# Kernel tuning notes

Measured on AMD Instinct MI355X. Metric: run time of the kernel, lower is better.

The kernel has to match this reference:

```python
import jax, jax.numpy as jnp
import numpy as np

N_NODES = 100000
N_EDGES = 3200000
N_FEAT = 128
EMBED = 20
N_CLASSES = 10
N_GRAPHS = 64


def setup_inputs() -> dict:
    key = jax.random.key(0)
    ks = jax.random.split(key, 8)
    x = jax.random.normal(ks[0], (N_NODES, N_FEAT), dtype=jnp.float32)
    edge_index = jax.random.randint(ks[1], (2, N_EDGES), 0, N_NODES, dtype=jnp.int64)
    edge_weights = jax.random.uniform(ks[2], (N_EDGES,), dtype=jnp.float32)
    batch = jnp.sort(jax.random.randint(ks[3], (N_NODES,), 0, N_GRAPHS, dtype=jnp.int64))
    # GCNConv parameters (glorot-ish scale) and final linear layer
    W = jax.random.normal(ks[4], (N_FEAT, EMBED), dtype=jnp.float32) * (1.0 / np.sqrt(N_FEAT))
    b = jnp.zeros((EMBED,), dtype=jnp.float32)
    lin_W = jax.random.normal(ks[5], (2 * EMBED, N_CLASSES), dtype=jnp.float32) * (1.0 / np.sqrt(2 * EMBED))
    lin_b = jnp.zeros((N_CLASSES,), dtype=jnp.float32)
    return {"x": x, "edge_index": edge_index, "edge_weights": edge_weights,
            "batch": batch, "W": W, "b": b, "lin_W": lin_W, "lin_b": lin_b}


def reference(x, edge_index, edge_weights, batch, W, b, lin_W, lin_b):
    N = x.shape[0]
    # --- GCNConv with self-loops and symmetric normalization (PyG semantics) ---
    loops = jnp.arange(N, dtype=edge_index.dtype)
    src = jnp.concatenate([edge_index[0], loops])
    dst = jnp.concatenate([edge_index[1], loops])
    w = jnp.concatenate([edge_weights, jnp.ones((N,), dtype=edge_weights.dtype)])
    deg = jax.ops.segment_sum(w, dst, num_segments=N)  # degree at targets
    dinv = jnp.where(deg > 0, jax.lax.rsqrt(deg), 0.0)
    norm = dinv[src] * w * dinv[dst]  # [E+N]
    xw = x @ W  # [N, EMBED]
    msg = xw[src] * norm[:, None]  # gather + scale
    out1 = jax.ops.segment_sum(msg, dst, num_segments=N) + b  # scatter-add
    # --- L2 normalize per node (F.normalize p=2 dim=1, eps=1e-12), then ReLU ---
    nrm = jnp.sqrt(jnp.sum(out1 * out1, axis=1, keepdims=True))
    embed = jax.nn.relu(out1 / jnp.maximum(nrm, 1e-12))
    # --- global max / mean pool per graph ---
    mx = jax.ops.segment_max(embed, batch, num_segments=N_GRAPHS)
    mx = jnp.where(jnp.isfinite(mx), mx, 0.0)  # empty graphs -> 0
    cnt = jax.ops.segment_sum(jnp.ones((N,), dtype=embed.dtype), batch, num_segments=N_GRAPHS)
    mean = jax.ops.segment_sum(embed, batch, num_segments=N_GRAPHS) / jnp.maximum(cnt, 1.0)[:, None]
    pooled = jnp.concatenate([mx, mean], axis=-1)  # [G, 2*EMBED]
    return pooled @ lin_W + lin_b
```

## Files before the change

kernel.cpp:

```cpp
#include <hip/hip_runtime.h>
#include <hip/hip_fp16.h>

#define NN 100000
#define NE 3200000
#define NF 128
#define EM 20
#define NC 10
#define NG 64

#define NB 782
#define CAPB 4608
#define T 4096
#define SBLK 1024
#define NXW 391

__global__ __launch_bounds__(SBLK) void k_scatfat(
        const int* __restrict__ src, const int* __restrict__ dst,
        const float* __restrict__ w, int* __restrict__ gcursor,
        uint2* __restrict__ barr,
        const float* __restrict__ x, const float* __restrict__ W,
        float* __restrict__ xwf) {
    __shared__ __align__(16) char smem[52352];
    int tid = threadIdx.x;

    if (blockIdx.x < NXW) {
        float* Ws = (float*)smem;
        for (int i = tid; i < NF * EM; i += SBLK) Ws[i] = W[i];
        __syncthreads();
        int node = blockIdx.x * 256 + (tid >> 2);
        int j0 = (tid & 3) * 5;
        if (node >= NN) return;
        float acc[5] = {0.f, 0.f, 0.f, 0.f, 0.f};
        const float4* xr = (const float4*)(x + (size_t)node * NF);
        for (int k4 = 0; k4 < NF / 4; ++k4) {
            float4 xc = xr[k4];
            const float* wr = Ws + (k4 * 4) * EM + j0;
#pragma unroll
            for (int jj = 0; jj < 5; ++jj) acc[jj] = fmaf(xc.x, wr[jj], acc[jj]);
            wr += EM;
#pragma unroll
            for (int jj = 0; jj < 5; ++jj) acc[jj] = fmaf(xc.y, wr[jj], acc[jj]);
            wr += EM;
#pragma unroll
            for (int jj = 0; jj < 5; ++jj) acc[jj] = fmaf(xc.z, wr[jj], acc[jj]);
            wr += EM;
#pragma unroll
            for (int jj = 0; jj < 5; ++jj) acc[jj] = fmaf(xc.w, wr[jj], acc[jj]);
        }
        float* o = xwf + (size_t)node * EM + j0;
#pragma unroll
        for (int jj = 0; jj < 5; ++jj) o[jj] = acc[jj];
        return;
    }

    unsigned int* cnt   = (unsigned int*)smem;
    unsigned int* off   = (unsigned int*)(smem + 4096);
    unsigned int* gbase = (unsigned int*)(smem + 8192);
    unsigned int* wsum  = (unsigned int*)(smem + 11320);
    uint2*        staged= (uint2*)(smem + 11384);
    unsigned short* bkt = (unsigned short*)(smem + 44152);

    long E0 = (long)(blockIdx.x - NXW) * T;
    int tot = (int)min((long)T, (long)NE - E0);
    cnt[tid] = 0;
    __syncthreads();
    unsigned int dreg[T / SBLK];
#pragma unroll
    for (int k = 0; k < T / SBLK; ++k) {
        int e = k * SBLK + tid;
        dreg[k] = 0;
        if (e < tot) {
            dreg[k] = (unsigned)dst[E0 + e];
            atomicAdd(&cnt[dreg[k] >> 7], 1u);
        }
    }
    __syncthreads();
    {
        int lane = tid & 63, wv = tid >> 6;
        unsigned int v = cnt[tid];
        unsigned int s = v;
#pragma unroll
        for (int o = 1; o < 64; o <<= 1) {
            unsigned int t = __shfl_up(s, o);
            if (lane >= o) s += t;
        }
        if (lane == 63) wsum[wv] = s;
        __syncthreads();
        if (tid == 0) {
            unsigned int a = 0;
#pragma unroll
            for (int i = 0; i < 16; ++i) { unsigned int t = wsum[i]; wsum[i] = a; a += t; }
        }
        __syncthreads();
        off[tid] = wsum[wv] + s - v;
    }
    __syncthreads();
    if (tid < NB) {
        unsigned int c = cnt[tid];
        gbase[tid] = c ? (unsigned int)atomicAdd(&gcursor[tid], (int)c) : 0u;
        cnt[tid] = 0;
    }
    __syncthreads();
#pragma unroll
    for (int k = 0; k < T / SBLK; ++k) {
        int e = k * SBLK + tid;
        if (e < tot) {
            long ge = E0 + e;
            unsigned int d = dreg[k];
            unsigned int b = d >> 7;
            unsigned int slot = atomicAdd(&cnt[b], 1u);
            unsigned int pos = off[b] + slot;
            staged[pos] = make_uint2((((unsigned)src[ge]) << 7) | (d & 127u),
                                     __float_as_uint(w[ge]));
            bkt[pos] = (unsigned short)b;
        }
    }
    __syncthreads();
    for (int i = tid; i < tot; i += SBLK) {
        unsigned int b = bkt[i];
        unsigned int gpos = gbase[b] + ((unsigned)i - off[b]);
        if (gpos < CAPB) barr[(size_t)b * CAPB + gpos] = staged[i];
    }
}

__global__ __launch_bounds__(1024) void k_degps(
        const int* __restrict__ gcursor, const uint2* __restrict__ barr,
        const float* xwf, float* __restrict__ dinv,
        __half* __restrict__ xwhA, __half* __restrict__ xwhB) {
    __shared__ float dacc[128];
    __shared__ float dvs[128];
    int bk = blockIdx.x, tid = threadIdx.x;
    if (tid < 128) dacc[tid] = 0.f;
    __syncthreads();
    int cntb = min(gcursor[bk], CAPB);
    const uint2* row = barr + (size_t)bk * CAPB;
    for (int i = tid; i < cntb; i += 1024) {
        uint2 r = row[i];
        atomicAdd(&dacc[r.x & 127u], __uint_as_float(r.y));
    }
    __syncthreads();
    if (tid < 128) {
        float dv = rsqrtf(1.0f + dacc[tid]);
        dvs[tid] = dv;
        int gd = bk * 128 + tid;
        if (gd < NN) dinv[gd] = dv;
    }
    __syncthreads();
    for (int i = tid; i < 128 * EM; i += 1024) {
        int n = i / EM, dim = i - n * EM;
        int gd = bk * 128 + n;
        if (gd < NN) {
            __half hv = __float2half(xwf[(size_t)gd * EM + dim] * dvs[n]);
            if (dim < 16) xwhA[(size_t)gd * 16 + dim] = hv;
            else          xwhB[(size_t)gd * 4 + (dim - 16)] = hv;
        }
    }
}

__device__ inline void unpack16(uint4 a0, uint4 a1, float* f) {
    const __half2* h = (const __half2*)&a0;
#pragma unroll
    for (int c = 0; c < 4; ++c) { float2 t = __half22float2(h[c]); f[2*c] = t.x; f[2*c+1] = t.y; }
    h = (const __half2*)&a1;
#pragma unroll
    for (int c = 0; c < 4; ++c) { float2 t = __half22float2(h[c]); f[8+2*c] = t.x; f[9+2*c] = t.y; }
}
__device__ inline void unpack4(uint2 b0, float* f) {
    const __half2* h = (const __half2*)&b0;
#pragma unroll
    for (int c = 0; c < 2; ++c) { float2 t = __half22float2(h[c]); f[2*c] = t.x; f[2*c+1] = t.y; }
}

__global__ void k_sortaggr(const int* __restrict__ gcursor,
                           const unsigned long long* __restrict__ barr64,
                           const __half* __restrict__ xwhA, const __half* __restrict__ xwhB,
                           const float* __restrict__ dinv, const float* __restrict__ b,
                           float* embed) {
    __shared__ unsigned long long srt[CAPB];
    __shared__ unsigned int cnt[128];
    __shared__ unsigned int off[128];
    __shared__ unsigned int wtot;
    int bk = blockIdx.x, tid = threadIdx.x;
    if (tid < 128) cnt[tid] = 0;
    __syncthreads();
    int cntb = min(gcursor[bk], CAPB);
    const unsigned long long* row = barr64 + (size_t)bk * CAPB;
    unsigned long long rec[9];
    unsigned int pos[9];
    int K = 0;
    for (int e = tid; e < cntb; e += 512) {
        rec[K] = row[e];
        pos[K] = atomicAdd(&cnt[(unsigned)rec[K] & 127u], 1u);
        ++K;
    }
    __syncthreads();
    unsigned int v = 0, s = 0;
    if (tid < 128) {
        v = cnt[tid]; s = v;
#pragma unroll
        for (int o = 1; o < 64; o <<= 1) {
            unsigned int t = __shfl_up(s, o);
            if ((tid & 63) >= o) s += t;
        }
        if (tid == 63) wtot = s;
    }
    __syncthreads();
    if (tid < 128) {
        if (tid >= 64) s += wtot;
        off[tid] = s;
    }
    __syncthreads();
    for (int k = 0; k < K; ++k) {
        unsigned int dl = (unsigned)rec[k] & 127u;
        srt[off[dl] - cnt[dl] + pos[k]] = rec[k];
    }
    __syncthreads();
    int d = tid >> 2, sub = tid & 3;
    int s0 = (int)(off[d] - cnt[d]), s1 = (int)off[d];
    const uint4* pA = (const uint4*)xwhA;
    const uint2* pB = (const uint2*)xwhB;
    float acc[20];
#pragma unroll
    for (int j = 0; j < 20; ++j) acc[j] = 0.f;
    for (int e = s0 + sub; e < s1; e += 4) {
        unsigned long long r = srt[e];
        unsigned int sN = ((unsigned int)r) >> 7;
        float nw = __uint_as_float((unsigned int)(r >> 32));
        uint4 a0 = pA[(size_t)sN * 2];
        uint4 a1 = pA[(size_t)sN * 2 + 1];
        uint2 b0 = pB[sN];
        float f[20];
        unpack16(a0, a1, f);
        unpack4(b0, f + 16);
#pragma unroll
        for (int j = 0; j < 20; ++j) acc[j] = fmaf(f[j], nw, acc[j]);
    }
#pragma unroll
    for (int j = 0; j < 20; ++j) {
        acc[j] += __shfl_xor(acc[j], 1);
        acc[j] += __shfl_xor(acc[j], 2);
    }
    if (sub == 0) {
        int gd = bk * 128 + d;
        if (gd < NN) {
            float dv = dinv[gd];
            uint4 a0 = pA[(size_t)gd * 2];
            uint4 a1 = pA[(size_t)gd * 2 + 1];
            uint2 b0 = pB[gd];
            float xdh[20];
            unpack16(a0, a1, xdh);
            unpack4(b0, xdh + 16);
            float r[20];
            float ss = 0.f;
#pragma unroll
            for (int j = 0; j < 20; ++j) {
                r[j] = dv * (acc[j] + xdh[j]) + b[j];
                ss = fmaf(r[j], r[j], ss);
            }
            float inv = 1.0f / fmaxf(sqrtf(ss), 1e-12f);
            float4 o4[5];
            float* o = (float*)o4;
#pragma unroll
            for (int j = 0; j < 20; ++j) {
                float e2 = r[j] * inv;
                o[j] = e2 > 0.f ? e2 : 0.f;
            }
            float4* eo = (float4*)(embed + (size_t)gd * EM);
#pragma unroll
            for (int c = 0; c < 5; ++c) eo[c] = o4[c];
        }
    }
}

__device__ inline int lbound(const int* __restrict__ batch, int key) {
    int lo = 0, hi = NN;
    while (lo < hi) {
        int mid = (lo + hi) >> 1;
        if (batch[mid] < key) lo = mid + 1; else hi = mid;
    }
    return lo;
}

__global__ void k_poolfinal(const float* __restrict__ embed, const int* __restrict__ batch,
                            const float* __restrict__ lw, const float* __restrict__ lb,
                            float* __restrict__ out) {
    __shared__ float cross[4][40];
    __shared__ float pooled[40];
    int g = blockIdx.x;
    int s0 = lbound(batch, g), s1 = lbound(batch, g + 1);
    int cnt = s1 - s0;
    float mx[EM], sm[EM];
#pragma unroll
    for (int j = 0; j < EM; ++j) { mx[j] = 0.f; sm[j] = 0.f; }
    for (int n = s0 + threadIdx.x; n < s1; n += 256) {
        const float4* e = (const float4*)(embed + (size_t)n * EM);
#pragma unroll
        for (int c = 0; c < 5; ++c) {
            float4 v = e[c];
            int j = c * 4;
            mx[j+0] = fmaxf(mx[j+0], v.x); sm[j+0] += v.x;
            mx[j+1] = fmaxf(mx[j+1], v.y); sm[j+1] += v.y;
            mx[j+2] = fmaxf(mx[j+2], v.z); sm[j+2] += v.z;
            mx[j+3] = fmaxf(mx[j+3], v.w); sm[j+3] += v.w;
        }
    }
#pragma unroll
    for (int o = 32; o > 0; o >>= 1) {
#pragma unroll
        for (int j = 0; j < EM; ++j) {
            mx[j] = fmaxf(mx[j], __shfl_xor(mx[j], o));
            sm[j] += __shfl_xor(sm[j], o);
        }
    }
    int wave = threadIdx.x >> 6, lane = threadIdx.x & 63;
    if (lane == 0) {
#pragma unroll
        for (int j = 0; j < EM; ++j) { cross[wave][j] = mx[j]; cross[wave][EM + j] = sm[j]; }
    }
    __syncthreads();
    if (threadIdx.x < 40) {
        int j = threadIdx.x;
        float v = cross[0][j];
        if (j < EM) v = fmaxf(fmaxf(v, cross[1][j]), fmaxf(cross[2][j], cross[3][j]));
        else        v = v + cross[1][j] + cross[2][j] + cross[3][j];
        if (j >= EM) v *= 1.0f / fmaxf((float)cnt, 1.0f);
        pooled[j] = v;
    }
    __syncthreads();
    if (threadIdx.x < NC) {
        int c = threadIdx.x;
        float acc = lb[c];
#pragma unroll
        for (int j = 0; j < 2 * EM; ++j) acc = fmaf(pooled[j], lw[j * NC + c], acc);
        out[g * NC + c] = acc;
    }
}

static inline size_t align_up(size_t v) { return (v + 1023) & ~(size_t)1023; }

extern "C" void kernel_launch(void* const* d_in, const int* in_sizes, int n_in,
                              void* d_out, int out_size, void* d_ws, size_t ws_size,
                              hipStream_t stream) {
    const float* x     = (const float*)d_in[0];
    const int*   ei    = (const int*)d_in[1];
    const float* ew    = (const float*)d_in[2];
    const int*   batch = (const int*)d_in[3];
    const float* W     = (const float*)d_in[4];
    const float* b     = (const float*)d_in[5];
    const float* lw    = (const float*)d_in[6];
    const float* lb    = (const float*)d_in[7];
    float* out = (float*)d_out;

    char* ws = (char*)d_ws;
    int*    gcursor = (int*)ws;    ws += align_up(4096);
    float*  dinv    = (float*)ws;  ws += align_up((size_t)NN * 4);
    __half* xwhA    = (__half*)ws; ws += align_up((size_t)NN * 16 * 2);
    __half* xwhB    = (__half*)ws; ws += align_up((size_t)NN * 4 * 2);
    float*  xwf     = (float*)ws;  ws += align_up((size_t)NN * EM * 4);
    uint2*  barr    = (uint2*)ws;
    unsigned long long* barr64 = (unsigned long long*)barr;
    float*  embed   = xwf;

    const int* srcp = ei;
    const int* dstp = ei + NE;

    (void)hipMemsetAsync(gcursor, 0, 4096, stream);
    k_scatfat<<<NXW + (NE + T - 1) / T, SBLK, 0, stream>>>(srcp, dstp, ew, gcursor, barr,
                                                           x, W, xwf);
    k_degps<<<NB, 1024, 0, stream>>>(gcursor, barr, xwf, dinv, xwhA, xwhB);
    k_sortaggr<<<NB, 512, 0, stream>>>(gcursor, barr64, xwhA, xwhB, dinv, b, embed);
    k_poolfinal<<<NG, 256, 0, stream>>>(embed, batch, lw, lb, out);
}
```

Measured before the change: 238.4 us.

## Fuse global max/mean pooling into aggregation kernel via shared-memory atomics

The per-node embedding is no longer written to global memory. The aggregation kernel now accumulates per-graph sums, counts and maxima in shared memory, using the int bit pattern of non-negative floats for atomicMax, then flushes them to small global buffers with atomics. A tiny final kernel computes the means and the linear layer. This removes the 8 MB embed write and re-read and the binary-search pooling kernel, at the cost of many LDS atomics per node and non-deterministic float summation order.

```diff
diff --git a/kernel.cpp b/kernel.cpp
--- a/kernel.cpp
+++ b/kernel.cpp
@@ -13,6 +13,7 @@
 #define T 4096
 #define SBLK 1024
 #define NXW 391
+#define GSPAN 16
 
 __global__ __launch_bounds__(SBLK) void k_scatfat(
         const int* __restrict__ src, const int* __restrict__ dst,
@@ -125,7 +126,7 @@
 
 __global__ __launch_bounds__(1024) void k_degps(
         const int* __restrict__ gcursor, const uint2* __restrict__ barr,
-        const float* xwf, float* __restrict__ dinv,
+        const float* __restrict__ xwf, float* __restrict__ dinv,
         __half* __restrict__ xwhA, __half* __restrict__ xwhB) {
     __shared__ float dacc[128];
     __shared__ float dvs[128];
@@ -175,13 +176,22 @@
                            const unsigned long long* __restrict__ barr64,
                            const __half* __restrict__ xwhA, const __half* __restrict__ xwhB,
                            const float* __restrict__ dinv, const float* __restrict__ b,
-                           float* embed) {
+                           const int* __restrict__ batch,
+                           float* __restrict__ gsum, int* __restrict__ gmaxI,
+                           int* __restrict__ gcnt) {
     __shared__ unsigned long long srt[CAPB];
     __shared__ unsigned int cnt[128];
     __shared__ unsigned int off[128];
     __shared__ unsigned int wtot;
+    __shared__ float lsum[GSPAN][EM];
+    __shared__ int   lmaxI[GSPAN][EM];
+    __shared__ int   lcnt[GSPAN];
+    __shared__ int   gmin_s;
     int bk = blockIdx.x, tid = threadIdx.x;
     if (tid < 128) cnt[tid] = 0;
+    for (int i = tid; i < GSPAN * EM; i += 512) { lsum[i / EM][i % EM] = 0.f; lmaxI[i / EM][i % EM] = 0; }
+    if (tid < GSPAN) lcnt[tid] = 0;
+    if (tid == 0) gmin_s = batch[bk * 128];
     __syncthreads();
     int cntb = min(gcursor[bk], CAPB);
     const unsigned long long* row = barr64 + (size_t)bk * CAPB;
@@ -258,81 +268,63 @@
                 ss = fmaf(r[j], r[j], ss);
             }
             float inv = 1.0f / fmaxf(sqrtf(ss), 1e-12f);
-            float4 o4[5];
-            float* o = (float*)o4;
+            float o[20];
 #pragma unroll
             for (int j = 0; j < 20; ++j) {
                 float e2 = r[j] * inv;
                 o[j] = e2 > 0.f ? e2 : 0.f;
             }
-            float4* eo = (float4*)(embed + (size_t)gd * EM);
-#pragma unroll
-            for (int c = 0; c < 5; ++c) eo[c] = o4[c];
-        }
-    }
-}
-
-__device__ inline int lbound(const int* __restrict__ batch, int key) {
-    int lo = 0, hi = NN;
-    while (lo < hi) {
-        int mid = (lo + hi) >> 1;
-        if (batch[mid] < key) lo = mid + 1; else hi = mid;
-    }
-    return lo;
-}
-
-__global__ void k_poolfinal(const float* __restrict__ embed, const int* __restrict__ batch,
-                            const float* __restrict__ lw, const float* __restrict__ lb,
-                            float* __restrict__ out) {
-    __shared__ float cross[4][40];
-    __shared__ float pooled[40];
-    int g = blockIdx.x;
-    int s0 = lbound(batch, g), s1 = lbound(batch, g + 1);
-    int cnt = s1 - s0;
-    float mx[EM], sm[EM];
-#pragma unroll
-    for (int j = 0; j < EM; ++j) { mx[j] = 0.f; sm[j] = 0.f; }
-    for (int n = s0 + threadIdx.x; n < s1; n += 256) {
-        const float4* e = (const float4*)(embed + (size_t)n * EM);
-#pragma unroll
-        for (int c = 0; c < 5; ++c) {
-            float4 v = e[c];
-            int j = c * 4;
-            mx[j+0] = fmaxf(mx[j+0], v.x); sm[j+0] += v.x;
-            mx[j+1] = fmaxf(mx[j+1], v.y); sm[j+1] += v.y;
-            mx[j+2] = fmaxf(mx[j+2], v.z); sm[j+2] += v.z;
-            mx[j+3] = fmaxf(mx[j+3], v.w); sm[j+3] += v.w;
-        }
-    }
-#pragma unroll
-    for (int o = 32; o > 0; o >>= 1) {
-#pragma unroll
-        for (int j = 0; j < EM; ++j) {
-            mx[j] = fmaxf(mx[j], __shfl_xor(mx[j], o));
-            sm[j] += __shfl_xor(sm[j], o);
-        }
-    }
-    int wave = threadIdx.x >> 6, lane = threadIdx.x & 63;
-    if (lane == 0) {
-#pragma unroll
-        for (int j = 0; j < EM; ++j) { cross[wave][j] = mx[j]; cross[wave][EM + j] = sm[j]; }
-    }
-    __syncthreads();
-    if (threadIdx.x < 40) {
-        int j = threadIdx.x;
-        float v = cross[0][j];
-        if (j < EM) v = fmaxf(fmaxf(v, cross[1][j]), fmaxf(cross[2][j], cross[3][j]));
-        else        v = v + cross[1][j] + cross[2][j] + cross[3][j];
-        if (j >= EM) v *= 1.0f / fmaxf((float)cnt, 1.0f);
-        pooled[j] = v;
-    }
-    __syncthreads();
-    if (threadIdx.x < NC) {
-        int c = threadIdx.x;
-        float acc = lb[c];
-#pragma unroll
-        for (int j = 0; j < 2 * EM; ++j) acc = fmaf(pooled[j], lw[j * NC + c], acc);
-        out[g * NC + c] = acc;
+            int g = batch[gd];
+            int gl = g - gmin_s;
+            if (gl < GSPAN) {
+#pragma unroll
+                for (int j = 0; j < 20; ++j) {
+                    atomicAdd(&lsum[gl][j], o[j]);
+                    atomicMax(&lmaxI[gl][j], __float_as_int(o[j]));
+                }
+                atomicAdd(&lcnt[gl], 1);
+            } else {
+#pragma unroll
+                for (int j = 0; j < 20; ++j) {
+                    atomicAdd(&gsum[g * EM + j], o[j]);
+                    atomicMax(&gmaxI[g * EM + j], __float_as_int(o[j]));
+                }
+                atomicAdd(&gcnt[g], 1);
+            }
+        }
+    }
+    __syncthreads();
+    for (int i = tid; i < GSPAN * EM; i += 512) {
+        int gl = i / EM, j = i - gl * EM;
+        int g = gmin_s + gl;
+        if (g < NG && lcnt[gl] > 0) {
+            atomicAdd(&gsum[g * EM + j], lsum[gl][j]);
+            atomicMax(&gmaxI[g * EM + j], lmaxI[gl][j]);
+        }
+    }
+    if (tid < GSPAN) {
+        int g = gmin_s + tid;
+        if (g < NG && lcnt[tid] > 0) atomicAdd(&gcnt[g], lcnt[tid]);
+    }
+}
+
+__global__ void k_final(const float* __restrict__ gsum, const int* __restrict__ gmaxI,
+                        const int* __restrict__ gcnt,
+                        const float* __restrict__ lw, const float* __restrict__ lb,
+                        float* __restrict__ out) {
+    __shared__ float pooled[2 * EM];
+    int g = blockIdx.x, tid = threadIdx.x;
+    if (tid < EM) pooled[tid] = __int_as_float(gmaxI[g * EM + tid]);
+    else if (tid < 2 * EM) {
+        float c = (float)gcnt[g];
+        pooled[tid] = gsum[g * EM + (tid - EM)] / fmaxf(c, 1.0f);
+    }
+    __syncthreads();
+    if (tid < NC) {
+        float acc = lb[tid];
+#pragma unroll
+        for (int j = 0; j < 2 * EM; ++j) acc = fmaf(pooled[j], lw[j * NC + tid], acc);
+        out[g * NC + tid] = acc;
     }
 }
 
@@ -353,21 +345,25 @@
 
     char* ws = (char*)d_ws;
     int*    gcursor = (int*)ws;    ws += align_up(4096);
+    char*   poolws  = ws;          ws += align_up(5120 + 5120 + 256);
+    float*  gsum    = (float*)poolws;
+    int*    gmaxI   = (int*)(poolws + 5120);
+    int*    gcnt    = (int*)(poolws + 10240);
     float*  dinv    = (float*)ws;  ws += align_up((size_t)NN * 4);
     __half* xwhA    = (__half*)ws; ws += align_up((size_t)NN * 16 * 2);
     __half* xwhB    = (__half*)ws; ws += align_up((size_t)NN * 4 * 2);
     float*  xwf     = (float*)ws;  ws += align_up((size_t)NN * EM * 4);
     uint2*  barr    = (uint2*)ws;
     unsigned long long* barr64 = (unsigned long long*)barr;
-    float*  embed   = xwf;
 
     const int* srcp = ei;
     const int* dstp = ei + NE;
 
-    (void)hipMemsetAsync(gcursor, 0, 4096, stream);
+    (void)hipMemsetAsync(gcursor, 0, align_up(4096) + align_up(10496), stream);
     k_scatfat<<<NXW + (NE + T - 1) / T, SBLK, 0, stream>>>(srcp, dstp, ew, gcursor, barr,
                                                            x, W, xwf);
     k_degps<<<NB, 1024, 0, stream>>>(gcursor, barr, xwf, dinv, xwhA, xwhB);
-    k_sortaggr<<<NB, 512, 0, stream>>>(gcursor, barr64, xwhA, xwhB, dinv, b, embed);
-    k_poolfinal<<<NG, 256, 0, stream>>>(embed, batch, lw, lb, out);
-}
+    k_sortaggr<<<NB, 512, 0, stream>>>(gcursor, barr64, xwhA, xwhB, dinv, b,
+                                       batch, gsum, gmaxI, gcnt);
+    k_final<<<NG, 64, 0, stream>>>(gsum, gmaxI, gcnt, lw, lb, out);
+}
```

After: 232.4 us (median of 2 runs). -2.5%, faster.
